# Kernel tuning notes

Measured on AMD Instinct MI355X. Metric: run time of the kernel, lower is better.

Reference implementation:

```python
import jax, jax.numpy as jnp
import numpy as np

B, C, Hh, Ww = 32, 512, 6, 40
NC = 97   # num classes; padding_idx = NC-1, start_idx = NC-2
L = 26    # label length (max_len+1); decoder tokens T = L+1 = 27


def _lstm2(x, layers):
    """2-layer unidirectional LSTM, batch_first, PyTorch gate order (i,f,g,o).
    x: (B,T,D); layers: list of (Wih, Whh, bih, bhh). Returns (B,T,H)."""
    h = x
    for (Wih, Whh, bih, bhh) in layers:
        Hd = Whh.shape[1]
        b = bih + bhh
        def step(carry, xt, Wih=Wih, Whh=Whh, b=b):
            hh, cc = carry
            g = xt @ Wih.T + hh @ Whh.T + b
            i, f, gg, o = jnp.split(g, 4, axis=-1)
            cc = jax.nn.sigmoid(f) * cc + jax.nn.sigmoid(i) * jnp.tanh(gg)
            hh = jax.nn.sigmoid(o) * jnp.tanh(cc)
            return (hh, cc), hh
        init = (jnp.zeros((h.shape[0], Hd), h.dtype), jnp.zeros((h.shape[0], Hd), h.dtype))
        _, ys = jax.lax.scan(step, init, jnp.swapaxes(h, 0, 1))
        h = jnp.swapaxes(ys, 0, 1)
    return h


def setup_inputs() -> dict:
    key = jax.random.key(0)
    it = iter(jax.random.split(key, 48))
    def nrm(shape, s=0.02):
        return jax.random.normal(next(it), shape, jnp.float32) * s
    d = {}
    d['feat'] = jax.random.normal(next(it), (B, C, Hh, Ww), jnp.float32)
    d['label'] = jax.random.randint(next(it), (B, L), 0, NC)
    d['valid_ratios'] = jax.random.uniform(next(it), (B,), jnp.float32, 0.5, 1.0)
    # encoder LSTM (2 layers, 512->512)
    for p in ['e0', 'e1']:
        d[p + '_Wih'] = nrm((4 * C, C)); d[p + '_Whh'] = nrm((4 * C, C))
        d[p + '_bih'] = jnp.zeros((4 * C,), jnp.float32); d[p + '_bhh'] = jnp.zeros((4 * C,), jnp.float32)
    d['enc_W'] = nrm((C, C)); d['enc_b'] = jnp.zeros((C,), jnp.float32)
    # attention: query 1x1 (Linear), key conv3x3, score 1x1 (Linear d->1)
    d['q_W'] = nrm((C, C)); d['q_b'] = jnp.zeros((C,), jnp.float32)
    d['k_W'] = nrm((C, C, 3, 3)); d['k_b'] = jnp.zeros((C,), jnp.float32)
    d['s_W'] = nrm((1, C)); d['s_b'] = jnp.zeros((1,), jnp.float32)
    emb = nrm((NC, C), 1.0)
    d['emb'] = emb.at[NC - 1].set(0.0)  # padding_idx row is zero
    # decoder LSTM (2 layers, 512->512)
    for p in ['d0', 'd1']:
        d[p + '_Wih'] = nrm((4 * C, C)); d[p + '_Whh'] = nrm((4 * C, C))
        d[p + '_bih'] = jnp.zeros((4 * C,), jnp.float32); d[p + '_bhh'] = jnp.zeros((4 * C,), jnp.float32)
    d['pred_W'] = nrm((NC, 3 * C)); d['pred_b'] = jnp.zeros((NC,), jnp.float32)
    return d


def reference(feat, label, valid_ratios,
              e0_Wih, e0_Whh, e0_bih, e0_bhh, e1_Wih, e1_Whh, e1_bih, e1_bhh,
              enc_W, enc_b, q_W, q_b, k_W, k_b, s_W, s_b, emb,
              d0_Wih, d0_Whh, d0_bih, d0_bhh, d1_Wih, d1_Whh, d1_bih, d1_bhh,
              pred_W, pred_b):
    # --- SAREncoder: max-pool over height, 2-layer LSTM, linear on last step ---
    feat_v = jnp.max(feat, axis=2).transpose(0, 2, 1)  # (B, W, C)
    hf = _lstm2(feat_v, [(e0_Wih, e0_Whh, e0_bih, e0_bhh), (e1_Wih, e1_Whh, e1_bih, e1_bhh)])
    holistic = hf[:, -1, :] @ enc_W.T + enc_b  # (B, C)
    # --- tokens: [holistic, embed(label)] ---
    tok = jnp.concatenate([holistic[:, None, :], emb[label]], axis=1)  # (B, T=L+1, C)
    Hid = _lstm2(tok, [(d0_Wih, d0_Whh, d0_bih, d0_bhh), (d1_Wih, d1_Whh, d1_bih, d1_bhh)])
    # --- 2D additive attention ---
    q = Hid @ q_W.T + q_b  # (B, T, C)
    k = jax.lax.conv_general_dilated(feat, k_W, (1, 1), 'SAME',
                                     dimension_numbers=('NCHW', 'OIHW', 'NCHW')) + k_b[None, :, None, None]
    t = jnp.tanh(k[:, None] + q[:, :, :, None, None])  # (B, T, C, h, w) big intermediate
    score = jnp.einsum('btchw,c->bthw', t, s_W[0]) + s_b[0]  # (B, T, h, w)
    vw = jnp.minimum(Ww, jnp.ceil(Ww * valid_ratios)).astype(jnp.int32)  # (B,)
    colmask = jnp.arange(Ww)[None, :] >= vw[:, None]  # (B, w)
    score = jnp.where(colmask[:, None, None, :], -jnp.inf, score)
    T = score.shape[1]
    aw = jax.nn.softmax(score.reshape(score.shape[0], T, -1), axis=-1).reshape(score.shape[0], T, Hh, Ww)
    attn_feat = jnp.einsum('bchw,bthw->btc', feat, aw)  # (B, T, C)
    # --- prediction (pred_concat=True); dropout is identity (deterministic) ---
    hol = jnp.broadcast_to(holistic[:, None, :], Hid.shape)
    preds = jnp.concatenate([Hid, attn_feat, hol], axis=-1) @ pred_W.T + pred_b
    return preds[:, 1:, :]  # (B, L, NC)
```

## Files before the change

kernel.cpp:

```cpp
#include <hip/hip_runtime.h>

typedef unsigned short u16;
typedef __attribute__((ext_vector_type(8))) short short8;
typedef __attribute__((ext_vector_type(4))) float floatx4;
typedef _Float16 half8 __attribute__((ext_vector_type(8)));
typedef _Float16 half2v __attribute__((ext_vector_type(2)));
typedef unsigned uint4v __attribute__((ext_vector_type(4)));

#define AGENT __HIP_MEMORY_SCOPE_AGENT
#define SENT 0x7FFF7FFFu

__device__ __forceinline__ float bf2f(u16 v) { return __uint_as_float(((unsigned)v) << 16); }
__device__ __forceinline__ u16 f2bf(float f) {
    unsigned u = __float_as_uint(f);
    unsigned r = (u + 0x7FFFu + ((u >> 16) & 1u)) >> 16;
    return (u16)r;
}
__device__ __forceinline__ float sigm_(float x) {
    return __builtin_amdgcn_rcpf(1.f + __expf(-x));
}
__device__ __forceinline__ float tanh_(float x) {
    x = fminf(fmaxf(x, -15.f), 15.f);
    float e = __expf(2.f * x);
    return (e - 1.f) * __builtin_amdgcn_rcpf(e + 1.f);
}

typedef __attribute__((address_space(1))) void gvoid_t;
typedef __attribute__((address_space(3))) void lvoid_t;
__device__ __forceinline__ void gl_lds16(const void* g, void* l) {
    __builtin_amdgcn_global_load_lds((gvoid_t*)g, (lvoid_t*)l, 16, 0, 0);
}

#define HEX_WORDS (134 * 32 * 256)

__global__ void init_k(const void* __restrict__ feat_raw, int* __restrict__ flag,
                       unsigned* __restrict__ hEx) {
    int idx = blockIdx.x * 256 + threadIdx.x;
    hEx[idx] = SENT;
    if (idx == 0) {
        const u16* p = (const u16*)feat_raw;
        int insane = 0;
        #pragma unroll
        for (int i = 0; i < 32; i += 2) {
            float x = bf2f(p[i]);
            float a = fabsf(x);
            if (!(a <= 1000.f)) insane = 1;
            if (x != 0.f && a < 1e-8f) insane = 1;
        }
        *flag = insane;
    }
}

struct SrcPtrs {
    const void* e0Wih; const void* e1Wih; const void* d0Wih; const void* d1Wih;
    const void* b0; const void* b1; const void* b2; const void* b3;
    const void* b4; const void* b5; const void* b6; const void* b7;
    const void* encW; const void* qW; const void* predW; const void* emb;
    const void* encb; const void* qb; const void* kb; const void* sW;
    const void* sb; const void* predb;
};
#define OFF_W0      0
#define OFF_W1      1048576
#define OFF_W2      2097152
#define OFF_W3      3145728
#define OFF_B       4194304
#define OFF_ENCW    4210688
#define OFF_QW      4472832
#define OFF_PREDW   4734976
#define OFF_EMB     4883968
#define OFF_ENCB    4933632
#define OFF_QB      4934144
#define OFF_KB      4934656
#define OFF_SW      4935168
#define OFF_SB      4935680
#define OFF_PREDB   4935681
#define CANON_TOTAL 4935778

__global__ __launch_bounds__(256) void canon_all(SrcPtrs S, u16* __restrict__ dst,
                                                 const int* __restrict__ flag) {
    int idx = blockIdx.x * 256 + threadIdx.x;
    if (idx >= CANON_TOTAL) return;
    const void* s; int loc;
    if (idx < OFF_B) {
        int k = idx >> 20; loc = idx & 1048575;
        s = (k == 0) ? S.e0Wih : (k == 1) ? S.e1Wih : (k == 2) ? S.d0Wih : S.d1Wih;
    } else if (idx < OFF_ENCW) {
        int r = idx - OFF_B; int k = r >> 11; loc = r & 2047;
        s = (k == 0) ? S.b0 : (k == 1) ? S.b1 : (k == 2) ? S.b2 : (k == 3) ? S.b3
          : (k == 4) ? S.b4 : (k == 5) ? S.b5 : (k == 6) ? S.b6 : S.b7;
    } else if (idx < OFF_QW)    { s = S.encW;  loc = idx - OFF_ENCW; }
    else if (idx < OFF_PREDW)   { s = S.qW;    loc = idx - OFF_QW; }
    else if (idx < OFF_EMB)     { s = S.predW; loc = idx - OFF_PREDW; }
    else if (idx < OFF_ENCB)    { s = S.emb;   loc = idx - OFF_EMB; }
    else if (idx < OFF_QB)      { s = S.encb;  loc = idx - OFF_ENCB; }
    else if (idx < OFF_KB)      { s = S.qb;    loc = idx - OFF_QB; }
    else if (idx < OFF_SW)      { s = S.kb;    loc = idx - OFF_KB; }
    else if (idx < OFF_SB)      { s = S.sW;    loc = idx - OFF_SW; }
    else if (idx < OFF_PREDB)   { s = S.sb;    loc = idx - OFF_SB; }
    else                        { s = S.predb; loc = idx - OFF_PREDB; }
    dst[idx] = (*flag) ? f2bf(((const float*)s)[loc]) : ((const u16*)s)[loc];
}

__global__ __launch_bounds__(64) void canonf_k(const void* __restrict__ src, float* __restrict__ dst,
                                               int n, const int* __restrict__ flag) {
    int i = blockIdx.x * 64 + threadIdx.x;
    if (i >= n) return;
    dst[i] = (*flag) ? ((const float*)src)[i] : bf2f(((const u16*)src)[i]);
}

__device__ __forceinline__ float rdf(const void* p, long i, int fl) {
    return fl ? ((const float*)p)[i] : bf2f(((const u16*)p)[i]);
}

__global__ __launch_bounds__(256) void featv_k(const void* __restrict__ feat, u16* __restrict__ featv,
                                               const int* __restrict__ flag) {
    const int fl = *flag;
    int idx = blockIdx.x * 256 + threadIdx.x;
    int c = idx & 511;
    int r = idx >> 9;
    int w = r % 40, b = r / 40;
    float mx = -1e30f;
    long base = ((long)(b * 512 + c) * 6) * 40 + w;
    #pragma unroll
    for (int h = 0; h < 6; h++) mx = fmaxf(mx, rdf(feat, base + h * 40, fl));
    featv[idx] = f2bf(mx);
}

__global__ __launch_bounds__(256) void padfeat_k(const void* __restrict__ feat, u16* __restrict__ featP,
                                                 const int* __restrict__ flag) {
    const int fl = *flag;
    int idx = blockIdx.x * 256 + threadIdx.x;
    int c = idx & 511;
    int r = idx >> 9;
    int wp = r % 42; int r2 = r / 42;
    int hp = r2 & 7; int b = r2 >> 3;
    u16 v = 0;
    if (hp >= 1 && hp <= 6 && wp >= 1 && wp <= 40) {
        long si = ((long)(b * 512 + c) * 6 + (hp - 1)) * 40 + (wp - 1);
        v = fl ? f2bf(((const float*)feat)[si]) : ((const u16*)feat)[si];
    }
    featP[idx] = v;
}

__global__ __launch_bounds__(256) void w2_k(const void* __restrict__ kW, u16* __restrict__ W2,
                                            const int* __restrict__ flag) {
    int idx = blockIdx.x * 256 + threadIdx.x;
    int co = idx / 4608;
    int r = idx % 4608;
    int kh = r / 1536;
    int r2 = r % 1536;
    int kw = r2 / 512;
    int ci = r2 & 511;
    long si = ((long)(co * 512 + ci) * 3 + kh) * 3 + kw;
    W2[idx] = (*flag) ? f2bf(((const float*)kW)[si]) : ((const u16*)kW)[si];
}

__global__ __launch_bounds__(256) void wq3_all(
    const void* __restrict__ s0, const void* __restrict__ s1,
    const void* __restrict__ s2, const void* __restrict__ s3,
    _Float16* __restrict__ d0, _Float16* __restrict__ d1,
    _Float16* __restrict__ d2, _Float16* __restrict__ d3,
    const int* __restrict__ flag)
{
    int gb = blockIdx.x;
    int id = gb >> 9;
    const void* W = (id == 0) ? s0 : (id == 1) ? s1 : (id == 2) ? s2 : s3;
    _Float16* D = (id == 0) ? d0 : (id == 1) ? d1 : (id == 2) ? d2 : d3;
    int o = (gb & 511) * 256 + threadIdx.x;
    int t = o & 511;
    int c = (o >> 9) & 31;
    int j = o >> 14;
    int rid = t >> 1, hf = t & 1;
    int n = (rid >> 6) * 512 + j * 64 + (rid & 63);
    int k = hf * 256 + c * 8;
    int fl = *flag;
    _Float16* dst = D + (long)o * 8;
    #pragma unroll
    for (int jj = 0; jj < 8; jj++) {
        long si = (long)n * 512 + k + jj;
        float v = fl ? ((const float*)W)[si] : bf2f(((const u16*)W)[si]);
        dst[jj] = (_Float16)v;
    }
}

__global__ __launch_bounds__(256) void gemm_nt_f32(
    const u16* __restrict__ A, int lda,
    const u16* __restrict__ Bw,
    const u16* __restrict__ bias0, const u16* __restrict__ bias1,
    float* __restrict__ C, int M, int N, int K, int ldc)
{
    __shared__ __align__(16) u16 As[64][40];
    __shared__ __align__(16) u16 Bs[64][40];
    const int tid = threadIdx.x;
    const int bn = blockIdx.x, bm = blockIdx.y;
    const int l = tid & 63, wid = tid >> 6;
    const int wm = wid >> 1, wn = wid & 1;
    const int lr = tid >> 2, lc = (tid & 3) * 8;
    const int l15 = l & 15, lq = l >> 4;

    floatx4 acc00 = (floatx4)(0.f), acc01 = (floatx4)(0.f), acc10 = (floatx4)(0.f), acc11 = (floatx4)(0.f);

    int am = bm * 64 + lr; if (am > M - 1) am = M - 1;
    const u16* Ap = A + (long)am * lda + lc;
    const u16* Bp = Bw + (long)(bn * 64 + lr) * K + lc;

    for (int k0 = 0; k0 < K; k0 += 32) {
        *(short8*)&As[lr][lc] = *(const short8*)(Ap + k0);
        *(short8*)&Bs[lr][lc] = *(const short8*)(Bp + k0);
        __syncthreads();
        short8 af0 = *(const short8*)&As[wm * 32 + l15][lq * 8];
        short8 af1 = *(const short8*)&As[wm * 32 + 16 + l15][lq * 8];
        short8 bf0 = *(const short8*)&Bs[wn * 32 + l15][lq * 8];
        short8 bf1 = *(const short8*)&Bs[wn * 32 + 16 + l15][lq * 8];
        acc00 = __builtin_amdgcn_mfma_f32_16x16x32_bf16(af0, bf0, acc00, 0, 0, 0);
        acc01 = __builtin_amdgcn_mfma_f32_16x16x32_bf16(af0, bf1, acc01, 0, 0, 0);
        acc10 = __builtin_amdgcn_mfma_f32_16x16x32_bf16(af1, bf0, acc10, 0, 0, 0);
        acc11 = __builtin_amdgcn_mfma_f32_16x16x32_bf16(af1, bf1, acc11, 0, 0, 0);
        __syncthreads();
    }
    floatx4 accs[2][2] = {{acc00, acc01}, {acc10, acc11}};
    #pragma unroll
    for (int i = 0; i < 2; i++)
        #pragma unroll
        for (int j = 0; j < 2; j++)
            #pragma unroll
            for (int r = 0; r < 4; r++) {
                int gm = bm * 64 + wm * 32 + i * 16 + lq * 4 + r;
                int gn = bn * 64 + wn * 32 + j * 16 + l15;
                if (gm < M) {
                    float v = accs[i][j][r];
                    if (bias0) v += bf2f(bias0[gn]);
                    if (bias1) v += bf2f(bias1[gn]);
                    C[(long)gm * ldc + gn] = v;
                }
            }
}

__global__ __launch_bounds__(512) void conv_gemm(
    const u16* __restrict__ featP, const u16* __restrict__ W2,
    const u16* __restrict__ kb, u16* __restrict__ kmap)
{
    __shared__ __align__(16) u16 As[4][128][32];
    __shared__ __align__(16) u16 Bs[4][128][32];
    const int tid = threadIdx.x;
    int bm = blockIdx.x * 8 + (blockIdx.y & 7);
    int bn = blockIdx.y >> 3;
    if (bm >= 60) return;
    const int wv = tid >> 6, l = tid & 63;
    const int wm = wv >> 2, wn = wv & 3;
    const int l15 = l & 15, lq = l >> 4;
    const int ch = ((l & 3) ^ ((l >> 3) & 3)) * 8;

    int ar = bm * 128 + wv * 16 + (l >> 2);
    int ab = ar / 240, ahw = ar % 240;
    const u16* ga = featP + ((long)(ab * 8 + ahw / 40) * 42 + (ahw % 40)) * 512 + ch;
    const u16* gb = W2 + (long)(bn * 128 + wv * 16 + (l >> 2)) * 4608 + ch;

    floatx4 acc[4][2];
    #pragma unroll
    for (int i = 0; i < 4; i++)
        #pragma unroll
        for (int j = 0; j < 2; j++) acc[i][j] = (floatx4)(0.f);

    auto stage = [&](int k0, int pb) {
        int kh = k0 / 1536;
        int rem = k0 - kh * 1536;
        int aoff = (kh * 42 + (rem >> 9)) * 512 + (rem & 511);
        gl_lds16(ga + aoff, &As[pb][wv * 16][0]);
        gl_lds16(gb + k0, &Bs[pb][wv * 16][0]);
    };

    const int rs = (lq ^ ((l15 >> 1) & 3)) * 8;

    auto compute = [&](int cur) {
        short8 af[4], bf[2];
        #pragma unroll
        for (int i = 0; i < 4; i++) af[i] = *(const short8*)&As[cur][wm * 64 + i * 16 + l15][rs];
        #pragma unroll
        for (int j = 0; j < 2; j++) bf[j] = *(const short8*)&Bs[cur][wn * 32 + j * 16 + l15][rs];
        #pragma unroll
        for (int i = 0; i < 4; i++)
            #pragma unroll
            for (int j = 0; j < 2; j++)
                acc[i][j] = __builtin_amdgcn_mfma_f32_16x16x32_bf16(af[i], bf[j], acc[i][j], 0, 0, 0);
    };

    stage(0, 0); stage(32, 1); stage(64, 2);
    for (int k = 0; k < 142; k++) {
        asm volatile("s_waitcnt vmcnt(4)" ::: "memory");
        __builtin_amdgcn_s_barrier();
        asm volatile("" ::: "memory");
        if (k < 141) stage((k + 3) * 32, (k + 3) & 3);
        compute(k & 3);
    }
    asm volatile("s_waitcnt vmcnt(2)" ::: "memory");
    __builtin_amdgcn_s_barrier();
    asm volatile("" ::: "memory");
    compute(2);
    asm volatile("s_waitcnt vmcnt(0)" ::: "memory");
    __builtin_amdgcn_s_barrier();
    asm volatile("" ::: "memory");
    compute(3);

    #pragma unroll
    for (int i = 0; i < 4; i++)
        #pragma unroll
        for (int j = 0; j < 2; j++)
            #pragma unroll
            for (int r = 0; r < 4; r++) {
                int row = bm * 128 + wm * 64 + i * 16 + lq * 4 + r;
                int col = bn * 128 + wn * 32 + j * 16 + l15;
                kmap[(long)row * 512 + col] = f2bf(acc[i][j][r] + bf2f(kb[col]));
            }
}

#define WL(F) F(0) F(1) F(2) F(3) F(4) F(5) F(6) F(7) F(8) F(9) F(10) F(11) F(12) F(13) F(14) F(15) \
              F(16) F(17) F(18) F(19) F(20) F(21) F(22) F(23) F(24) F(25) F(26) F(27) F(28) F(29) F(30) F(31)
#define WLA(F) F(0,0) F(1,1) F(2,2) F(3,3) F(4,0) F(5,1) F(6,2) F(7,3) \
               F(8,0) F(9,1) F(10,2) F(11,3) F(12,0) F(13,1) F(14,2) F(15,3) \
               F(16,0) F(17,1) F(18,2) F(19,3) F(20,0) F(21,1) F(22,2) F(23,3) \
               F(24,0) F(25,1) F(26,2) F(27,3) F(28,0) F(29,1) F(30,2) F(31,3)
#define WDECL(i) half8 w##i = wp8[(long)(j * 32 + i) * 512 + tid];
#define WPIN(i)  asm volatile("" : "+v"(w##i));
#define DOTC(i,k) { \
    half8 hv = *(const half8*)&hS2[(hf * 2 + (i / 16)) * 136 + (i % 16) * 8]; \
    a##k = __builtin_amdgcn_fdot2(__builtin_shufflevector(hv, hv, 0, 1), __builtin_shufflevector(w##i, w##i, 0, 1), a##k, false); \
    a##k = __builtin_amdgcn_fdot2(__builtin_shufflevector(hv, hv, 2, 3), __builtin_shufflevector(w##i, w##i, 2, 3), a##k, false); \
    a##k = __builtin_amdgcn_fdot2(__builtin_shufflevector(hv, hv, 4, 5), __builtin_shufflevector(w##i, w##i, 4, 5), a##k, false); \
    a##k = __builtin_amdgcn_fdot2(__builtin_shufflevector(hv, hv, 6, 7), __builtin_shufflevector(w##i, w##i, 6, 7), a##k, false); }

__global__ __launch_bounds__(512) __attribute__((amdgpu_waves_per_eu(2, 2))) void lstm_sync(
    const float* __restrict__ xpre, const _Float16* __restrict__ Wq3,
    u16* __restrict__ seq_out, float* __restrict__ f32_out,
    unsigned* __restrict__ hExT, int T, int f32_ld)
{
    const int i_ = blockIdx.x;
    const int slot = i_ >> 3;
    const int b = (i_ & 7) * 4 + (slot & 3);
    const int j = slot >> 2;
    const int tid = threadIdx.x;
    const int hf = tid & 1;

    __shared__ __align__(16) _Float16 hS2[4 * 136];
    __shared__ float part[512];

    const half8* wp8 = (const half8*)Wq3;
    WL(WDECL)
    WL(WPIN)
    float cst = 0.f;

    for (int t = 0; t < T; t++) {
        float xi = 0.f, xf = 0.f, xg = 0.f, xo = 0.f;
        if (tid < 64) {
            const float* xp = xpre + ((long)b * T + t) * 2048 + j * 64 + tid;
            xi = xp[0]; xf = xp[512]; xg = xp[1024]; xo = xp[1536];
        }
        float a0 = 0.f, a1 = 0.f, a2 = 0.f, a3 = 0.f;
        if (t > 0) {
            if (tid < 64) {
                const unsigned* src = &hExT[((long)(t - 1) * 32 + b) * 256 + tid * 4];
                unsigned v0, v1, v2, v3;
                do {
                    v0 = __hip_atomic_load(src + 0, __ATOMIC_RELAXED, AGENT);
                    v1 = __hip_atomic_load(src + 1, __ATOMIC_RELAXED, AGENT);
                    v2 = __hip_atomic_load(src + 2, __ATOMIC_RELAXED, AGENT);
                    v3 = __hip_atomic_load(src + 3, __ATOMIC_RELAXED, AGENT);
                } while (v0 == SENT || v1 == SENT || v2 == SENT || v3 == SENT);
                uint4v v; v.x = v0; v.y = v1; v.z = v2; v.w = v3;
                *(uint4v*)&hS2[(tid >> 4) * 136 + (tid & 15) * 8] = v;
            }
            __syncthreads();
            WLA(DOTC)
        }
        part[tid] = (a0 + a1) + (a2 + a3);
        __syncthreads();
        if (tid < 64) {
            float gi = xi + part[(0   + tid) * 2] + part[(0   + tid) * 2 + 1];
            float gf = xf + part[(64  + tid) * 2] + part[(64  + tid) * 2 + 1];
            float gg = xg + part[(128 + tid) * 2] + part[(128 + tid) * 2 + 1];
            float go = xo + part[(192 + tid) * 2] + part[(192 + tid) * 2 + 1];
            cst = sigm_(gf) * cst + sigm_(gi) * tanh_(gg);
            float h = sigm_(go) * tanh_(cst);
            float hlo = __shfl(h, tid * 2);
            float hhi = __shfl(h, tid * 2 + 1);
            if (t + 1 < T && tid < 32) {
                half2v hp; hp[0] = (_Float16)hlo; hp[1] = (_Float16)hhi;
                __hip_atomic_store(&hExT[((long)t * 32 + b) * 256 + j * 32 + tid],
                                   *(unsigned*)&hp, __ATOMIC_RELAXED, AGENT);
            }
            asm volatile("" ::: "memory");
            long so = ((long)b * T + t) * 512 + j * 64 + tid;
            seq_out[so] = f2bf(h);
            if (f32_out) f32_out[((long)b * T + t) * f32_ld + j * 64 + tid] = h;
        }
    }
}

__global__ __launch_bounds__(256) void tok_k(
    const float* __restrict__ holf, const u16* __restrict__ cemb,
    const int* __restrict__ label, u16* __restrict__ tok)
{
    int idx = blockIdx.x * 256 + threadIdx.x;
    int c = idx & 511;
    int m = idx >> 9;
    int b = m / 27, t = m % 27;
    float v;
    if (t == 0) v = holf[(long)b * 512 + c];
    else v = bf2f(cemb[(long)label[b * 26 + (t - 1)] * 512 + c]);
    tok[idx] = f2bf(v);
}

__global__ __launch_bounds__(256) void score_k(
    const float* __restrict__ q, const u16* __restrict__ kmap,
    const u16* __restrict__ sW, const u16* __restrict__ sb,
    const float* __restrict__ vr, float* __restrict__ aw)
{
    int blk = blockIdx.x;
    int xcd = blk & 7, rest = blk >> 3;
    int bq = rest & 3, t = rest >> 2;
    int b = xcd * 4 + bq;
    int bt = b * 27 + t;
    int tid = threadIdx.x, wv = tid >> 6, ln = tid & 63;

    __shared__ float sc[240];
    __shared__ float red[256];

    float qr[8], sr[8];
    const float* qp = q + (long)bt * 512 + ln * 8;
    #pragma unroll
    for (int i = 0; i < 8; i++) qr[i] = qp[i];
    #pragma unroll
    for (int i = 0; i < 8; i++) sr[i] = bf2f(sW[ln * 8 + i]);

    const u16* kb_ = kmap + (long)b * 240 * 512;
    for (int r = wv * 60; r < wv * 60 + 60; r++) {
        short8 kv = *(const short8*)(kb_ + (long)r * 512 + ln * 8);
        float acc = 0.f;
        #pragma unroll
        for (int i = 0; i < 8; i++) {
            float x = bf2f((u16)kv[i]) + qr[i];
            acc = fmaf(sr[i], tanh_(x), acc);
        }
        #pragma unroll
        for (int m = 32; m > 0; m >>= 1) acc += __shfl_xor(acc, m);
        if (ln == 0) sc[r] = acc;
    }
    __syncthreads();

    float scv = -INFINITY, ex = 0.f;
    if (tid < 240) {
        float rr = vr[b];
        int vw = (int)ceilf(40.f * rr);
        if (vw > 40) vw = 40;
        int wcol = tid % 40;
        scv = (wcol >= vw) ? -INFINITY : (sc[tid] + bf2f(sb[0]));
    }
    red[tid] = scv;
    __syncthreads();
    for (int s = 128; s > 0; s >>= 1) {
        if (tid < s) red[tid] = fmaxf(red[tid], red[tid + s]);
        __syncthreads();
    }
    float mx = red[0];
    __syncthreads();
    if (tid < 240) ex = (scv == -INFINITY) ? 0.f : __expf(scv - mx);
    red[tid] = ex;
    __syncthreads();
    for (int s = 128; s > 0; s >>= 1) {
        if (tid < s) red[tid] += red[tid + s];
        __syncthreads();
    }
    float inv = __builtin_amdgcn_rcpf(red[0]);
    if (tid < 240) aw[(long)bt * 240 + tid] = ex * inv;
}

__global__ __launch_bounds__(256) void attn_k(
    const void* __restrict__ feat, const float* __restrict__ aw,
    float* __restrict__ concat, const int* __restrict__ flag)
{
    const int fl = *flag;
    int b = blockIdx.x >> 3;
    int cc = (blockIdx.x & 7) * 64;
    int tid = threadIdx.x;
    __shared__ float awS[27 * 240];
    __shared__ u16 fS[64 * 240];
    for (int i = tid; i < 27 * 240; i += 256) awS[i] = aw[(long)b * 27 * 240 + i];
    long fbase = ((long)b * 512 + cc) * 240;
    for (int i = tid; i < 64 * 240; i += 256)
        fS[i] = fl ? f2bf(((const float*)feat)[fbase + i]) : ((const u16*)feat)[fbase + i];
    __syncthreads();
    for (int item = tid; item < 64 * 27; item += 256) {
        int c = item / 27, t = item % 27;
        const u16* fp = &fS[c * 240];
        const float* ap = &awS[t * 240];
        float acc = 0.f;
        for (int hw = 0; hw < 240; hw++) acc = fmaf(bf2f(fp[hw]), ap[hw], acc);
        concat[((long)(b * 27 + t)) * 1536 + 512 + cc + c] = acc;
    }
}

__global__ __launch_bounds__(256) void pred_k(
    const float* __restrict__ concat, const float* __restrict__ holf,
    const u16* __restrict__ pW, const u16* __restrict__ pb,
    void* __restrict__ out, const int* __restrict__ flag)
{
    int m0 = blockIdx.x * 4;
    int tid = threadIdx.x;
    const int fl = *flag;
    __shared__ float aS[4][1024];
    __shared__ float hS[4][512];
    for (int i = tid; i < 4 * 1024; i += 256)
        aS[i / 1024][i % 1024] = concat[(long)(m0 + i / 1024) * 1536 + (i % 1024)];
    for (int i = tid; i < 4 * 512; i += 256) {
        int m = m0 + i / 512;
        hS[i / 512][i % 512] = holf[(long)(m / 27) * 512 + (i % 512)];
    }
    __syncthreads();
    int r = tid >> 6;
    int nb = tid & 63;
    int m = m0 + r;
    int b = m / 27, t = m % 27;
    for (int n = nb; n < 97; n += 64) {
        const u16* wp = pW + (long)n * 1536;
        float acc = 0.f;
        for (int k = 0; k < 1024; k++) acc = fmaf(aS[r][k], bf2f(wp[k]), acc);
        for (int k = 0; k < 512; k++) acc = fmaf(hS[r][k], bf2f(wp[1024 + k]), acc);
        acc += bf2f(pb[n]);
        if (t > 0) {
            long o = ((long)(b * 26 + (t - 1))) * 97 + n;
            if (fl) ((float*)out)[o] = acc;
            else    ((u16*)out)[o] = f2bf(acc);
        }
    }
}

extern "C" void kernel_launch(void* const* d_in, const int* in_sizes, int n_in,
                              void* d_out, int out_size, void* d_ws, size_t ws_size,
                              hipStream_t stream) {
    (void)in_sizes; (void)n_in; (void)out_size; (void)ws_size;
    const void* feat_r = d_in[0];
    const int*  label  = (const int*)d_in[1];
    const void* vr_r   = d_in[2];

    char* w = (char*)d_ws;
    size_t off = 0;
    auto alloc = [&](size_t bytes) -> void* {
        void* p = w + off;
        off = (off + bytes + 63) & ~(size_t)63;
        return p;
    };
    int*   flag    = (int*)  alloc(4);
    unsigned* hEx  = (unsigned*)alloc((size_t)HEX_WORDS * 4);
    u16*   canon   = (u16*)  alloc((size_t)CANON_TOTAL * 2);
    float* cvr     = (float*)alloc(32ull * 4);
    u16*   featv   = (u16*)  alloc(655360ull * 2);
    float* xpre    = (float*)alloc(2621440ull * 4);
    u16*   seq0    = (u16*)  alloc(655360ull * 2);
    u16*   seq1    = (u16*)  alloc(655360ull * 2);
    u16*   tok     = (u16*)  alloc(442368ull * 2);
    u16*   seqd0   = (u16*)  alloc(442368ull * 2);
    u16*   Hid     = (u16*)  alloc(442368ull * 2);
    float* holf    = (float*)alloc(16384ull * 4);
    float* qf      = (float*)alloc(442368ull * 4);
    u16*   featP   = (u16*)  alloc(5505024ull * 2);
    u16*   W2      = (u16*)  alloc(2359296ull * 2);
    float* aw      = (float*)alloc(207360ull * 4);
    float* concat  = (float*)alloc(1327104ull * 4);
    _Float16* Wq[4];
    for (int i = 0; i < 4; i++) Wq[i] = (_Float16*)alloc(1048576ull * 2);
    u16*   kmap    = (u16*)xpre;

    unsigned* hEx0 = hEx;
    unsigned* hEx1 = hEx + 40ull * 8192;
    unsigned* hEx2 = hEx + 80ull * 8192;
    unsigned* hEx3 = hEx + 107ull * 8192;

    u16* cW0    = canon + OFF_W0;
    u16* cW1    = canon + OFF_W1;
    u16* cW2    = canon + OFF_W2;
    u16* cW3    = canon + OFF_W3;
    u16* cb0    = canon + OFF_B;
    u16* cencW  = canon + OFF_ENCW;
    u16* cqW    = canon + OFF_QW;
    u16* cpredW = canon + OFF_PREDW;
    u16* cemb   = canon + OFF_EMB;
    u16* cencb  = canon + OFF_ENCB;
    u16* cqb    = canon + OFF_QB;
    u16* ckb    = canon + OFF_KB;
    u16* csW    = canon + OFF_SW;
    u16* csb    = canon + OFF_SB;
    u16* cpredb = canon + OFF_PREDB;

    init_k<<<dim3(HEX_WORDS / 256), 256, 0, stream>>>(feat_r, flag, hEx);
    SrcPtrs S;
    S.e0Wih = d_in[3];  S.e1Wih = d_in[7];  S.d0Wih = d_in[20]; S.d1Wih = d_in[24];
    S.b0 = d_in[5];  S.b1 = d_in[6];  S.b2 = d_in[9];  S.b3 = d_in[10];
    S.b4 = d_in[22]; S.b5 = d_in[23]; S.b6 = d_in[26]; S.b7 = d_in[27];
    S.encW = d_in[11]; S.qW = d_in[13]; S.predW = d_in[28]; S.emb = d_in[19];
    S.encb = d_in[12]; S.qb = d_in[14]; S.kb = d_in[16]; S.sW = d_in[17];
    S.sb = d_in[18]; S.predb = d_in[29];
    canon_all<<<dim3((CANON_TOTAL + 255) / 256), 256, 0, stream>>>(S, canon, flag);
    canonf_k<<<dim3(1), 64, 0, stream>>>(vr_r, cvr, 32, flag);
    w2_k<<<dim3(9216), 256, 0, stream>>>(d_in[15], W2, flag);
    wq3_all<<<dim3(2048), 256, 0, stream>>>(d_in[4], d_in[8], d_in[21], d_in[25],
                                            Wq[0], Wq[1], Wq[2], Wq[3], flag);

    featv_k  <<<dim3(2560), 256, 0, stream>>>(feat_r, featv, flag);
    padfeat_k<<<dim3(21504), 256, 0, stream>>>(feat_r, featP, flag);

    gemm_nt_f32<<<dim3(32, 20), 256, 0, stream>>>(featv, 512, cW0, cb0 + 0 * 2048, cb0 + 1 * 2048, xpre, 1280, 2048, 512, 2048);
    lstm_sync<<<dim3(256), 512, 0, stream>>>(xpre, Wq[0], seq0, nullptr, hEx0, 40, 0);
    gemm_nt_f32<<<dim3(32, 20), 256, 0, stream>>>(seq0, 512, cW1, cb0 + 2 * 2048, cb0 + 3 * 2048, xpre, 1280, 2048, 512, 2048);
    lstm_sync<<<dim3(256), 512, 0, stream>>>(xpre, Wq[1], seq1, nullptr, hEx1, 40, 0);
    gemm_nt_f32<<<dim3(8, 1), 256, 0, stream>>>(seq1 + 39 * 512, 40 * 512, cencW, cencb, nullptr, holf, 32, 512, 512, 512);

    tok_k<<<dim3(1728), 256, 0, stream>>>(holf, cemb, label, tok);
    gemm_nt_f32<<<dim3(32, 14), 256, 0, stream>>>(tok, 512, cW2, cb0 + 4 * 2048, cb0 + 5 * 2048, xpre, 864, 2048, 512, 2048);
    lstm_sync<<<dim3(256), 512, 0, stream>>>(xpre, Wq[2], seqd0, nullptr, hEx2, 27, 0);
    gemm_nt_f32<<<dim3(32, 14), 256, 0, stream>>>(seqd0, 512, cW3, cb0 + 6 * 2048, cb0 + 7 * 2048, xpre, 864, 2048, 512, 2048);
    lstm_sync<<<dim3(256), 512, 0, stream>>>(xpre, Wq[3], Hid, concat, hEx3, 27, 1536);

    gemm_nt_f32<<<dim3(8, 14), 256, 0, stream>>>(Hid, 512, cqW, cqb, nullptr, qf, 864, 512, 512, 512);
    conv_gemm<<<dim3(8, 32), 512, 0, stream>>>(featP, W2, ckb, kmap);
    score_k<<<dim3(864), 256, 0, stream>>>(qf, kmap, csW, csb, cvr, aw);
    attn_k<<<dim3(256), 256, 0, stream>>>(feat_r, aw, concat, flag);

    pred_k<<<dim3(216), 256, 0, stream>>>(concat, holf, cpredW, cpredb, d_out, flag);
}
```

Before: 815.6 us.

## Add 128x128-tile pipelined LDS-DMA GEMM for LSTM input and query projections

Adds a new GEMM kernel with 128x128 tiles and 512 threads. It uses a 4-stage ring of global-to-LDS direct loads with swizzled LDS addressing, and each wave computes a 64x32 sub-tile with bf16 MFMAs. The kernel replaces the 64x64 gemm_nt_f32 launches for the four LSTM input projections and the query projection, aiming for more operand reuse and for memory loads that overlap compute. It hardcodes K=512 and gives fewer blocks per launch, so small-M GEMMs use fewer CUs.

```diff
diff --git a/kernel.cpp b/kernel.cpp
--- a/kernel.cpp
+++ b/kernel.cpp
@@ -229,6 +229,85 @@
                 int gn = bn * 64 + wn * 32 + j * 16 + l15;
                 if (gm < M) {
                     float v = accs[i][j][r];
+                    if (bias0) v += bf2f(bias0[gn]);
+                    if (bias1) v += bf2f(bias1[gn]);
+                    C[(long)gm * ldc + gn] = v;
+                }
+            }
+}
+
+__global__ __launch_bounds__(512) void gemm_nt_128(
+    const u16* __restrict__ A, const u16* __restrict__ Bw,
+    const u16* __restrict__ bias0, const u16* __restrict__ bias1,
+    float* __restrict__ C, int M, int ldc)
+{
+    __shared__ __align__(16) u16 As[4][128][32];
+    __shared__ __align__(16) u16 Bs[4][128][32];
+    const int tid = threadIdx.x;
+    const int bn = blockIdx.x, bm = blockIdx.y;
+    const int wv = tid >> 6, l = tid & 63;
+    const int wm = wv >> 2, wn = wv & 3;
+    const int l15 = l & 15, lq = l >> 4;
+    const int ch = ((l & 3) ^ ((l >> 3) & 3)) * 8;
+
+    int ar = bm * 128 + wv * 16 + (l >> 2);
+    if (ar > M - 1) ar = M - 1;
+    const u16* ga = A + (long)ar * 512 + ch;
+    const u16* gb = Bw + (long)(bn * 128 + wv * 16 + (l >> 2)) * 512 + ch;
+
+    floatx4 acc[4][2];
+    #pragma unroll
+    for (int i = 0; i < 4; i++)
+        #pragma unroll
+        for (int j = 0; j < 2; j++) acc[i][j] = (floatx4)(0.f);
+
+    auto stage = [&](int k0, int pb) {
+        gl_lds16(ga + k0, &As[pb][wv * 16][0]);
+        gl_lds16(gb + k0, &Bs[pb][wv * 16][0]);
+    };
+
+    const int rs = (lq ^ ((l15 >> 1) & 3)) * 8;
+
+    auto compute = [&](int cur) {
+        short8 af[4], bf[2];
+        #pragma unroll
+        for (int i = 0; i < 4; i++) af[i] = *(const short8*)&As[cur][wm * 64 + i * 16 + l15][rs];
+        #pragma unroll
+        for (int j = 0; j < 2; j++) bf[j] = *(const short8*)&Bs[cur][wn * 32 + j * 16 + l15][rs];
+        #pragma unroll
+        for (int i = 0; i < 4; i++)
+            #pragma unroll
+            for (int j = 0; j < 2; j++)
+                acc[i][j] = __builtin_amdgcn_mfma_f32_16x16x32_bf16(af[i], bf[j], acc[i][j], 0, 0, 0);
+    };
+
+    stage(0, 0); stage(32, 1); stage(64, 2);
+    for (int k = 0; k < 14; k++) {
+        asm volatile("s_waitcnt vmcnt(4)" ::: "memory");
+        __builtin_amdgcn_s_barrier();
+        asm volatile("" ::: "memory");
+        if (k < 13) stage((k + 3) * 32, (k + 3) & 3);
+        compute(k & 3);
+    }
+    asm volatile("s_waitcnt vmcnt(2)" ::: "memory");
+    __builtin_amdgcn_s_barrier();
+    asm volatile("" ::: "memory");
+    compute(2);
+    asm volatile("s_waitcnt vmcnt(0)" ::: "memory");
+    __builtin_amdgcn_s_barrier();
+    asm volatile("" ::: "memory");
+    compute(3);
+
+    #pragma unroll
+    for (int i = 0; i < 4; i++)
+        #pragma unroll
+        for (int j = 0; j < 2; j++)
+            #pragma unroll
+            for (int r = 0; r < 4; r++) {
+                int gm = bm * 128 + wm * 64 + i * 16 + lq * 4 + r;
+                int gn = bn * 128 + wn * 32 + j * 16 + l15;
+                if (gm < M) {
+                    float v = acc[i][j][r];
                     if (bias0) v += bf2f(bias0[gn]);
                     if (bias1) v += bf2f(bias1[gn]);
                     C[(long)gm * ldc + gn] = v;
@@ -608,19 +687,19 @@
     featv_k  <<<dim3(2560), 256, 0, stream>>>(feat_r, featv, flag);
     padfeat_k<<<dim3(21504), 256, 0, stream>>>(feat_r, featP, flag);
 
-    gemm_nt_f32<<<dim3(32, 20), 256, 0, stream>>>(featv, 512, cW0, cb0 + 0 * 2048, cb0 + 1 * 2048, xpre, 1280, 2048, 512, 2048);
+    gemm_nt_128<<<dim3(16, 10), 512, 0, stream>>>(featv, cW0, cb0 + 0 * 2048, cb0 + 1 * 2048, xpre, 1280, 2048);
     lstm_sync<<<dim3(256), 512, 0, stream>>>(xpre, Wq[0], seq0, nullptr, hEx0, 40, 0);
-    gemm_nt_f32<<<dim3(32, 20), 256, 0, stream>>>(seq0, 512, cW1, cb0 + 2 * 2048, cb0 + 3 * 2048, xpre, 1280, 2048, 512, 2048);
+    gemm_nt_128<<<dim3(16, 10), 512, 0, stream>>>(seq0, cW1, cb0 + 2 * 2048, cb0 + 3 * 2048, xpre, 1280, 2048);
     lstm_sync<<<dim3(256), 512, 0, stream>>>(xpre, Wq[1], seq1, nullptr, hEx1, 40, 0);
     gemm_nt_f32<<<dim3(8, 1), 256, 0, stream>>>(seq1 + 39 * 512, 40 * 512, cencW, cencb, nullptr, holf, 32, 512, 512, 512);
 
     tok_k<<<dim3(1728), 256, 0, stream>>>(holf, cemb, label, tok);
-    gemm_nt_f32<<<dim3(32, 14), 256, 0, stream>>>(tok, 512, cW2, cb0 + 4 * 2048, cb0 + 5 * 2048, xpre, 864, 2048, 512, 2048);
+    gemm_nt_128<<<dim3(16, 7), 512, 0, stream>>>(tok, cW2, cb0 + 4 * 2048, cb0 + 5 * 2048, xpre, 864, 2048);
     lstm_sync<<<dim3(256), 512, 0, stream>>>(xpre, Wq[2], seqd0, nullptr, hEx2, 27, 0);
-    gemm_nt_f32<<<dim3(32, 14), 256, 0, stream>>>(seqd0, 512, cW3, cb0 + 6 * 2048, cb0 + 7 * 2048, xpre, 864, 2048, 512, 2048);
+    gemm_nt_128<<<dim3(16, 7), 512, 0, stream>>>(seqd0, cW3, cb0 + 6 * 2048, cb0 + 7 * 2048, xpre, 864, 2048);
     lstm_sync<<<dim3(256), 512, 0, stream>>>(xpre, Wq[3], Hid, concat, hEx3, 27, 1536);
 
-    gemm_nt_f32<<<dim3(8, 14), 256, 0, stream>>>(Hid, 512, cqW, cqb, nullptr, qf, 864, 512, 512, 512);
+    gemm_nt_128<<<dim3(4, 7), 512, 0, stream>>>(Hid, cqW, cqb, nullptr, qf, 864, 512);
     conv_gemm<<<dim3(8, 32), 512, 0, stream>>>(featP, W2, ckb, kmap);
     score_k<<<dim3(864), 256, 0, stream>>>(qf, kmap, csW, csb, cvr, aw);
     attn_k<<<dim3(256), 256, 0, stream>>>(feat_r, aw, concat, flag);
```

After: 819.7 us. About the same (+0.5%).
